# Kernel tuning notes

Measured on AMD Instinct MI355X. Metric: run time of the kernel, lower is better.

The kernel has to match this reference:

```python
import jax, jax.numpy as jnp
import numpy as np

B, A, G, C = 64, 8732, 50, 81
NEG_POS_RATIO = 3


def _make_boxes(key, b, n):
    k1, k2 = jax.random.split(key)
    mins = jax.random.uniform(k1, (b, n, 2)) * 0.7
    sizes = jax.random.uniform(k2, (b, n, 2)) * 0.3 + 0.01
    return jnp.concatenate([mins, mins + sizes], axis=-1)  # [b,n,4] xyxy


def setup_inputs() -> dict:
    key = jax.random.key(0)
    k1, k2, k3, k4 = jax.random.split(key, 4)
    pred_boxes = _make_boxes(k1, B, A)
    gt_boxes = _make_boxes(k2, B, G)
    pred_scores = jax.random.normal(k3, (B, A, C), dtype=jnp.float32)
    gt_labels = jax.random.randint(k4, (B, G), 0, C)
    return {"pred_boxes": pred_boxes, "pred_scores": pred_scores,
            "gt_boxes": gt_boxes, "gt_labels": gt_labels}


def _iou(a, b):
    # a: [B,A,4], b: [B,G,4] -> [B,A,G]
    a_ = a[:, :, None, :]
    b_ = b[:, None, :, :]
    iw = jnp.clip(jnp.minimum(a_[..., 2], b_[..., 2]) - jnp.maximum(a_[..., 0], b_[..., 0]), 0)
    ih = jnp.clip(jnp.minimum(a_[..., 3], b_[..., 3]) - jnp.maximum(a_[..., 1], b_[..., 1]), 0)
    inter = iw * ih
    area_a = (a_[..., 2] - a_[..., 0]) * (a_[..., 3] - a_[..., 1])
    area_b = (b_[..., 2] - b_[..., 0]) * (b_[..., 3] - b_[..., 1])
    union = jnp.clip(area_a + area_b - inter, 1e-6)
    return inter / union


def reference(pred_boxes, pred_scores, gt_boxes, gt_labels):
    num_anchors = pred_boxes.shape[1]
    iou = _iou(pred_boxes, gt_boxes)              # [B,A,G]
    best_iou = iou.max(axis=2)                    # [B,A]
    best_idx = iou.argmax(axis=2)                 # [B,A]
    pos = best_iou > 0.5

    matched_boxes = jnp.take_along_axis(gt_boxes, best_idx[..., None], axis=1)   # [B,A,4]
    matched_labels = jnp.take_along_axis(gt_labels, best_idx, axis=1)            # [B,A]
    target_boxes = jnp.where(pos[..., None], matched_boxes, 0.0)
    target_labels = jnp.where(pos, matched_labels, 0)

    pos_mask = target_labels > 0
    num_pos = pos_mask.sum(axis=1)                # [B]

    # smooth L1 (beta=1), summed over box coords
    d = pred_boxes - target_boxes
    ad = jnp.abs(d)
    sl1 = jnp.where(ad < 1.0, 0.5 * d * d, ad - 0.5).sum(axis=2)  # [B,A]
    loc_loss = (sl1 * pos_mask).sum()

    # cross entropy per anchor
    log_p = jax.nn.log_softmax(pred_scores, axis=-1)
    conf = -jnp.take_along_axis(log_p, target_labels[..., None], axis=-1)[..., 0]  # [B,A]

    conf_pos = (conf * pos_mask).sum()

    # hard negative mining: top (3*num_pos) losses among negatives
    conf_neg = jnp.where(pos_mask, -1.0, conf)
    num_neg = jnp.minimum(NEG_POS_RATIO * num_pos, num_anchors - 1)   # [B]
    order = jnp.argsort(-conf_neg, axis=1)        # descending
    rank = jnp.argsort(order, axis=1)             # rank of each anchor in sorted order
    hard_neg = rank < num_neg[:, None]
    conf_neg_hard = (conf * hard_neg).sum()

    total = (loc_loss + conf_pos + conf_neg_hard) / jnp.maximum(num_pos, 1).sum()
    return total
```

## Files before the change

kernel.cpp:

```cpp
#include <hip/hip_runtime.h>

#define BB 64
#define AA 8732
#define GG 50
#define CC 81
#define NEG_RATIO 3
#define HW 16
#define HSTRIDE 257
#define NCHUNK 137
#define XB 27


__device__ __forceinline__ unsigned mono_key(float f) {
    unsigned u = __float_as_uint(f);
    u = (u & 0x80000000u) ? ~u : (u | 0x80000000u);
    return ~u;
}

__device__ __forceinline__ float unkey_val(unsigned key) {
    unsigned u = ~key;
    return __uint_as_float((u & 0x80000000u) ? (u & 0x7fffffffu) : ~u);
}

__global__ __launch_bounds__(256, 5) void k_match(
    const float* __restrict__ pred_boxes, const float* __restrict__ pred_scores,
    const float* __restrict__ gt_boxes, const int* __restrict__ gt_labels,
    float* __restrict__ confneg_out,
    float* __restrict__ acc_slots, int* __restrict__ np_slots,
    unsigned* __restrict__ ctr)
{
    __shared__ float4 sgt[GG];
    __shared__ float  sarea[GG];
    __shared__ int    slab[GG];
    __shared__ float  redf[4];
    __shared__ int    redi[4];

    const int tid = threadIdx.x;
    const int b = blockIdx.y;
    const int x = blockIdx.x;
    const int grp = tid >> 2;
    const int q   = tid & 3;

    if (b == 0 && x == 0 && tid == 0) *ctr = 0u;

    if (tid < GG) {
        float4 g4 = ((const float4*)gt_boxes)[b * GG + tid];
        sgt[tid] = g4;
        sarea[tid] = (g4.z - g4.x) * (g4.w - g4.y);
        slab[tid] = gt_labels[b * GG + tid];
    }
    __syncthreads();

    const float*  sb = pred_scores + (size_t)b * AA * CC;
    const float4* bbx = (const float4*)pred_boxes + (size_t)b * AA;

    float contrib = 0.f;
    int npos = 0;

    const int a0 = x * 64 + grp;
    float4 cbox = bbx[a0];
    const float* crow = sb + (size_t)a0 * CC;
    float psum;
    {
        const float4 v0 = *(const float4*)(crow + 4 * q);
        const float4 v1 = *(const float4*)(crow + 4 * q + 16);
        const float4 v2 = *(const float4*)(crow + 4 * q + 32);
        const float4 v3 = *(const float4*)(crow + 4 * q + 48);
        const float4 v4 = *(const float4*)(crow + 4 * q + 64);
        const float  v80 = crow[80];
        float ps = 0.f;
        ps += __expf(v0.x) + __expf(v0.y) + __expf(v0.z) + __expf(v0.w);
        ps += __expf(v1.x) + __expf(v1.y) + __expf(v1.z) + __expf(v1.w);
        ps += __expf(v2.x) + __expf(v2.y) + __expf(v2.z) + __expf(v2.w);
        ps += __expf(v3.x) + __expf(v3.y) + __expf(v3.z) + __expf(v3.w);
        ps += __expf(v4.x) + __expf(v4.y) + __expf(v4.z) + __expf(v4.w);
        if (q == 0) ps += __expf(v80);
        psum = ps;
    }

    for (int c = x; c < NCHUNK; c += XB) {
        const int a = c * 64 + grp;
        const bool valid = a < AA;

        int cnx = c + XB; if (cnx >= NCHUNK) cnx = c;
        int an = cnx * 64 + grp; if (an >= AA) an = AA - 1;
        const float4 nbox = bbx[an];
        const float* nrow = sb + (size_t)an * CC;
        const float4 n0 = *(const float4*)(nrow + 4 * q);
        const float4 n1 = *(const float4*)(nrow + 4 * q + 16);
        const float4 n2 = *(const float4*)(nrow + 4 * q + 32);
        const float4 n3 = *(const float4*)(nrow + 4 * q + 48);
        const float4 n4 = *(const float4*)(nrow + 4 * q + 64);
        const float  n80 = nrow[80];

        const float4 pb = cbox;
        const float area_p = (pb.z - pb.x) * (pb.w - pb.y);
        float best = -1.f; int bidx = 0x7fffffff;
        #pragma unroll
        for (int i = 0; i < 13; ++i) {
            const int g = q + (i << 2);
            const bool gv = g < GG;
            const int gc = gv ? g : 0;
            const float4 gb = sgt[gc];
            const float  sa = sarea[gc];
            float iw = fmaxf(fminf(pb.z, gb.z) - fmaxf(pb.x, gb.x), 0.f);
            float ih = fmaxf(fminf(pb.w, gb.w) - fmaxf(pb.y, gb.y), 0.f);
            float inter = iw * ih;
            float uni = fmaxf(area_p + sa - inter, 1e-6f);
            float iou = __fdividef(inter, uni);
            if (gv && iou > best) { best = iou; bidx = g; }
        }
        #pragma unroll
        for (int off = 1; off < 4; off <<= 1) {
            float ov = __shfl_xor(best, off);
            int   oi = __shfl_xor(bidx, off);
            if (ov > best || (ov == best && oi < bidx)) { best = ov; bidx = oi; }
        }
        const int label = (best > 0.5f) ? slab[bidx] : 0;

        const float labv = crow[label];

        float sm = psum;
        sm += __shfl_xor(sm, 1);
        sm += __shfl_xor(sm, 2);

        if (q == 0 && valid) {
            const float conf = __logf(sm) - labv;
            const size_t ai = (size_t)b * AA + a;
            const bool pm = label > 0;
            confneg_out[ai] = pm ? -1.f : conf;
            if (pm) {
                npos++;
                const float4 gb = sgt[bidx];
                float sl1 = 0.f, d, ad;
                d = pb.x - gb.x; ad = fabsf(d); sl1 += (ad < 1.f) ? 0.5f * d * d : ad - 0.5f;
                d = pb.y - gb.y; ad = fabsf(d); sl1 += (ad < 1.f) ? 0.5f * d * d : ad - 0.5f;
                d = pb.z - gb.z; ad = fabsf(d); sl1 += (ad < 1.f) ? 0.5f * d * d : ad - 0.5f;
                d = pb.w - gb.w; ad = fabsf(d); sl1 += (ad < 1.f) ? 0.5f * d * d : ad - 0.5f;
                contrib += sl1 + conf;
            }
        }

        float ps = 0.f;
        ps += __expf(n0.x) + __expf(n0.y) + __expf(n0.z) + __expf(n0.w);
        ps += __expf(n1.x) + __expf(n1.y) + __expf(n1.z) + __expf(n1.w);
        ps += __expf(n2.x) + __expf(n2.y) + __expf(n2.z) + __expf(n2.w);
        ps += __expf(n3.x) + __expf(n3.y) + __expf(n3.z) + __expf(n3.w);
        ps += __expf(n4.x) + __expf(n4.y) + __expf(n4.z) + __expf(n4.w);
        if (q == 0) ps += __expf(n80);

        cbox = nbox; crow = nrow; psum = ps;
    }

    #pragma unroll
    for (int off = 32; off; off >>= 1) {
        contrib += __shfl_down(contrib, off);
        npos    += __shfl_down(npos, off);
    }
    const int wv = tid >> 6;
    if ((tid & 63) == 0) { redf[wv] = contrib; redi[wv] = npos; }
    __syncthreads();
    if (tid == 0) {
        acc_slots[b * XB + x] = redf[0] + redf[1] + redf[2] + redf[3];
        np_slots[b * XB + x]  = redi[0] + redi[1] + redi[2] + redi[3];
    }
}

__global__ __launch_bounds__(1024) void k_hardneg(
    const float* __restrict__ confneg,
    const int* __restrict__ np_slots, const float* __restrict__ acc_slots,
    float* __restrict__ per_b, int* __restrict__ den_b,
    unsigned* __restrict__ ctr, float* __restrict__ out)
{
    __shared__ unsigned hist[HW * HSTRIDE];
    __shared__ unsigned binsum[256];
    __shared__ unsigned sel[2];
    __shared__ unsigned uE[HW], uG[HW], eb[HW];
    __shared__ float    fred[HW];
    __shared__ int      stot;
    __shared__ int      slast;

    const int b = blockIdx.x;
    const int tid = threadIdx.x;
    const int wv = tid >> 6;
    const int lane = tid & 63;

    int np = 0;
    #pragma unroll
    for (int i = 0; i < XB; ++i) np += np_slots[b * XB + i];
    int k = NEG_RATIO * np; if (k > AA - 1) k = AA - 1;

    float hn = 0.f;
    if (k > 0) {
        const float* cn = confneg + (size_t)b * AA;

        const int lo = tid * 9;
        int nk = AA - lo; nk = nk > 9 ? 9 : (nk < 0 ? 0 : nk);
        unsigned keys[9];
        #pragma unroll
        for (int j = 0; j < 9; ++j)
            if (j < nk) keys[j] = mono_key(cn[lo + j]);

        unsigned prefix = 0, kk = (unsigned)k;
        for (int lev = 0; lev < 4; ++lev) {
            const int shift = 24 - 8 * lev;
            for (int i = tid; i < HW * HSTRIDE; i += 1024) hist[i] = 0;
            __syncthreads();
            #pragma unroll
            for (int j = 0; j < 9; ++j) {
                if (j < nk) {
                    const unsigned key = keys[j];
                    if (lev == 0 || (key >> (shift + 8)) == prefix)
                        atomicAdd(&hist[wv * HSTRIDE + ((key >> shift) & 255u)], 1u);
                }
            }
            __syncthreads();
            if (tid < 256) {
                unsigned s = 0;
                #pragma unroll
                for (int w = 0; w < HW; ++w) s += hist[w * HSTRIDE + tid];
                binsum[tid] = s;
            }
            __syncthreads();
            if (wv == 0) {
                const unsigned v0 = binsum[4 * lane], v1 = binsum[4 * lane + 1];
                const unsigned v2 = binsum[4 * lane + 2], v3 = binsum[4 * lane + 3];
                const unsigned lsum = v0 + v1 + v2 + v3;
                unsigned sc = lsum;
                #pragma unroll
                for (int off = 1; off < 64; off <<= 1) {
                    unsigned t = __shfl_up(sc, off);
                    if (lane >= off) sc += t;
                }
                const unsigned excl = sc - lsum;
                if (kk > excl && kk <= sc) {
                    unsigned cacc = excl;
                    if (kk <= cacc + v0)              { sel[0] = 4 * lane;     sel[1] = kk - cacc; }
                    else if (kk <= (cacc += v0) + v1) { sel[0] = 4 * lane + 1; sel[1] = kk - cacc; }
                    else if (kk <= (cacc += v1) + v2) { sel[0] = 4 * lane + 2; sel[1] = kk - cacc; }
                    else                              { sel[0] = 4 * lane + 3; sel[1] = kk - cacc - v2; }
                }
            }
            __syncthreads();
            prefix = (prefix << 8) | sel[0];
            kk = sel[1];
        }
        const unsigned kth = prefix;

        int cntG = 0, cntE = 0; float sum_gt = 0.f;
        #pragma unroll
        for (int j = 0; j < 9; ++j) {
            if (j < nk) {
                if (keys[j] < kth)       { cntG++; sum_gt += unkey_val(keys[j]); }
                else if (keys[j] == kth) { cntE++; }
            }
        }
        int sc = cntE;
        #pragma unroll
        for (int off = 1; off < 64; off <<= 1) {
            int t = __shfl_up(sc, off);
            if (lane >= off) sc += t;
        }
        int gt = cntG;
        #pragma unroll
        for (int off = 32; off; off >>= 1) gt += __shfl_down(gt, off);
        if (lane == 63) uE[wv] = (unsigned)sc;
        if (lane == 0)  uG[wv] = (unsigned)gt;
        __syncthreads();
        if (wv == 0) {
            unsigned e = (lane < HW) ? uE[lane] : 0u;
            unsigned g = (lane < HW) ? uG[lane] : 0u;
            unsigned se = e;
            #pragma unroll
            for (int off = 1; off < 16; off <<= 1) {
                unsigned t = __shfl_up(se, off);
                if (lane >= off) se += t;
            }
            if (lane < HW) eb[lane] = se - e;
            #pragma unroll
            for (int off = 8; off; off >>= 1) g += __shfl_down(g, off);
            if (lane == 0) stot = (int)g;
        }
        __syncthreads();
        const int m = k - stot;
        const int exclE = (int)eb[wv] + (sc - cntE);

        float sum_eq = 0.f;
        if (m > 0 && cntE > 0) {
            int seen = 0;
            #pragma unroll
            for (int j = 0; j < 9; ++j) {
                if (j < nk && keys[j] == kth) {
                    if (exclE + seen < m) sum_eq += unkey_val(keys[j]);
                    seen++;
                }
            }
        }

        float contrib = sum_gt + sum_eq;
        #pragma unroll
        for (int off = 32; off; off >>= 1) contrib += __shfl_down(contrib, off);
        if (lane == 0) fred[wv] = contrib;
        __syncthreads();
        if (tid == 0) {
            #pragma unroll
            for (int w = 0; w < HW; ++w) hn += fred[w];
        }
    }

    if (tid == 0) {
        float accb = 0.f;
        #pragma unroll
        for (int i = 0; i < XB; ++i) accb += acc_slots[b * XB + i];
        atomicExch(&per_b[b], accb + hn);
        atomicExch(&den_b[b], np > 1 ? np : 1);
        __threadfence();
        unsigned prev = atomicAdd(ctr, 1u);
        slast = (prev == (unsigned)(BB - 1)) ? 1 : 0;
    }
    __syncthreads();
    if (slast && tid < BB) {
        float v = atomicAdd(&per_b[tid], 0.f);
        int   d = atomicAdd(&den_b[tid], 0);
        #pragma unroll
        for (int off = 32; off; off >>= 1) {
            v += __shfl_down(v, off);
            d += __shfl_down(d, off);
        }
        if (tid == 0) out[0] = v / (float)d;
    }
}

extern "C" void kernel_launch(void* const* d_in, const int* in_sizes, int n_in,
                              void* d_out, int out_size, void* d_ws, size_t ws_size,
                              hipStream_t stream) {
    const float* pred_boxes  = (const float*)d_in[0];
    const float* pred_scores = (const float*)d_in[1];
    const float* gt_boxes    = (const float*)d_in[2];
    const int*   gt_labels   = (const int*)d_in[3];

    float*    ws        = (float*)d_ws;
    float*    acc_slots = ws;
    int*      np_slots  = (int*)(ws + 2048);
    float*    per_b     = ws + 4096;
    int*      den_b     = (int*)(ws + 4160);
    unsigned* ctr       = (unsigned*)(ws + 4224);
    float*    conf_neg  = ws + 8192;

    dim3 g1(XB, BB);
    k_match<<<g1, 256, 0, stream>>>(pred_boxes, pred_scores, gt_boxes, gt_labels,
                                    conf_neg, acc_slots, np_slots, ctr);
    k_hardneg<<<BB, 1024, 0, stream>>>(conf_neg, np_slots, acc_slots,
                                       per_b, den_b, ctr, (float*)d_out);
}
```

Measured before the change: 348.4 us.

## Split fused match kernel into separate log-sum-exp and IoU-matching kernels

Replaces the persistent, software-pipelined match kernel with two kernels. The first computes per-anchor log-sum-exp over the 81 classes with one block per 64-anchor chunk across the whole grid, storing it alongside the class-0 score. The second does IoU matching with one thread per anchor over all 50 ground-truth boxes, reading the stored LSE and gathering the label score only for positives. The aim is more parallelism and less register pressure per kernel, at the cost of an extra launch and a round trip of the intermediate LSE array through memory.

```diff
diff --git a/kernel.cpp b/kernel.cpp
--- a/kernel.cpp
+++ b/kernel.cpp
@@ -7,8 +7,7 @@
 #define NEG_RATIO 3
 #define HW 16
 #define HSTRIDE 257
-#define NCHUNK 137
-#define XB 27
+#define NXB 35
 
 
 __device__ __forceinline__ unsigned mono_key(float f) {
@@ -22,12 +21,51 @@
     return __uint_as_float((u & 0x80000000u) ? (u & 0x7fffffffu) : ~u);
 }
 
-__global__ __launch_bounds__(256, 5) void k_match(
+__global__ __launch_bounds__(256) void k_expsum(
+    const float* __restrict__ pred_scores,
+    float2* __restrict__ lse_s0, unsigned* __restrict__ ctr)
+{
+    const int tid = threadIdx.x;
+    const int b = blockIdx.y;
+    const int x = blockIdx.x;
+    const int grp = tid >> 2;
+    const int q   = tid & 3;
+
+    if (b == 0 && x == 0 && tid == 0) *ctr = 0u;
+
+    const int a = x * 64 + grp;
+    const int am = a < AA ? a : AA - 1;
+    const float* row = pred_scores + ((size_t)b * AA + am) * CC;
+
+    const float4 v0 = *(const float4*)(row + 4 * q);
+    const float4 v1 = *(const float4*)(row + 4 * q + 16);
+    const float4 v2 = *(const float4*)(row + 4 * q + 32);
+    const float4 v3 = *(const float4*)(row + 4 * q + 48);
+    const float4 v4 = *(const float4*)(row + 4 * q + 64);
+    const float  v80 = row[80];
+
+    float ps = 0.f;
+    ps += __expf(v0.x) + __expf(v0.y) + __expf(v0.z) + __expf(v0.w);
+    ps += __expf(v1.x) + __expf(v1.y) + __expf(v1.z) + __expf(v1.w);
+    ps += __expf(v2.x) + __expf(v2.y) + __expf(v2.z) + __expf(v2.w);
+    ps += __expf(v3.x) + __expf(v3.y) + __expf(v3.z) + __expf(v3.w);
+    ps += __expf(v4.x) + __expf(v4.y) + __expf(v4.z) + __expf(v4.w);
+    if (q == 0) ps += __expf(v80);
+
+    float sm = ps;
+    sm += __shfl_xor(sm, 1);
+    sm += __shfl_xor(sm, 2);
+
+    if (q == 0 && a < AA)
+        lse_s0[(size_t)b * AA + a] = make_float2(__logf(sm), v0.x);
+}
+
+__global__ __launch_bounds__(256) void k_iou(
     const float* __restrict__ pred_boxes, const float* __restrict__ pred_scores,
     const float* __restrict__ gt_boxes, const int* __restrict__ gt_labels,
+    const float2* __restrict__ lse_s0,
     float* __restrict__ confneg_out,
-    float* __restrict__ acc_slots, int* __restrict__ np_slots,
-    unsigned* __restrict__ ctr)
+    float* __restrict__ acc_slots, int* __restrict__ np_slots)
 {
     __shared__ float4 sgt[GG];
     __shared__ float  sarea[GG];
@@ -38,10 +76,6 @@
     const int tid = threadIdx.x;
     const int b = blockIdx.y;
     const int x = blockIdx.x;
-    const int grp = tid >> 2;
-    const int q   = tid & 3;
-
-    if (b == 0 && x == 0 && tid == 0) *ctr = 0u;
 
     if (tid < GG) {
         float4 g4 = ((const float4*)gt_boxes)[b * GG + tid];
@@ -51,105 +85,43 @@
     }
     __syncthreads();
 
-    const float*  sb = pred_scores + (size_t)b * AA * CC;
-    const float4* bbx = (const float4*)pred_boxes + (size_t)b * AA;
-
+    const int a = x * 256 + tid;
     float contrib = 0.f;
     int npos = 0;
 
-    const int a0 = x * 64 + grp;
-    float4 cbox = bbx[a0];
-    const float* crow = sb + (size_t)a0 * CC;
-    float psum;
-    {
-        const float4 v0 = *(const float4*)(crow + 4 * q);
-        const float4 v1 = *(const float4*)(crow + 4 * q + 16);
-        const float4 v2 = *(const float4*)(crow + 4 * q + 32);
-        const float4 v3 = *(const float4*)(crow + 4 * q + 48);
-        const float4 v4 = *(const float4*)(crow + 4 * q + 64);
-        const float  v80 = crow[80];
-        float ps = 0.f;
-        ps += __expf(v0.x) + __expf(v0.y) + __expf(v0.z) + __expf(v0.w);
-        ps += __expf(v1.x) + __expf(v1.y) + __expf(v1.z) + __expf(v1.w);
-        ps += __expf(v2.x) + __expf(v2.y) + __expf(v2.z) + __expf(v2.w);
-        ps += __expf(v3.x) + __expf(v3.y) + __expf(v3.z) + __expf(v3.w);
-        ps += __expf(v4.x) + __expf(v4.y) + __expf(v4.z) + __expf(v4.w);
-        if (q == 0) ps += __expf(v80);
-        psum = ps;
-    }
-
-    for (int c = x; c < NCHUNK; c += XB) {
-        const int a = c * 64 + grp;
-        const bool valid = a < AA;
-
-        int cnx = c + XB; if (cnx >= NCHUNK) cnx = c;
-        int an = cnx * 64 + grp; if (an >= AA) an = AA - 1;
-        const float4 nbox = bbx[an];
-        const float* nrow = sb + (size_t)an * CC;
-        const float4 n0 = *(const float4*)(nrow + 4 * q);
-        const float4 n1 = *(const float4*)(nrow + 4 * q + 16);
-        const float4 n2 = *(const float4*)(nrow + 4 * q + 32);
-        const float4 n3 = *(const float4*)(nrow + 4 * q + 48);
-        const float4 n4 = *(const float4*)(nrow + 4 * q + 64);
-        const float  n80 = nrow[80];
-
-        const float4 pb = cbox;
+    if (a < AA) {
+        const float4 pb = ((const float4*)pred_boxes)[(size_t)b * AA + a];
         const float area_p = (pb.z - pb.x) * (pb.w - pb.y);
-        float best = -1.f; int bidx = 0x7fffffff;
-        #pragma unroll
-        for (int i = 0; i < 13; ++i) {
-            const int g = q + (i << 2);
-            const bool gv = g < GG;
-            const int gc = gv ? g : 0;
-            const float4 gb = sgt[gc];
-            const float  sa = sarea[gc];
+        float best = -1.f; int bidx = 0;
+        #pragma unroll
+        for (int g = 0; g < GG; ++g) {
+            const float4 gb = sgt[g];
+            const float  sa = sarea[g];
             float iw = fmaxf(fminf(pb.z, gb.z) - fmaxf(pb.x, gb.x), 0.f);
             float ih = fmaxf(fminf(pb.w, gb.w) - fmaxf(pb.y, gb.y), 0.f);
             float inter = iw * ih;
             float uni = fmaxf(area_p + sa - inter, 1e-6f);
             float iou = __fdividef(inter, uni);
-            if (gv && iou > best) { best = iou; bidx = g; }
-        }
-        #pragma unroll
-        for (int off = 1; off < 4; off <<= 1) {
-            float ov = __shfl_xor(best, off);
-            int   oi = __shfl_xor(bidx, off);
-            if (ov > best || (ov == best && oi < bidx)) { best = ov; bidx = oi; }
+            if (iou > best) { best = iou; bidx = g; }
         }
         const int label = (best > 0.5f) ? slab[bidx] : 0;
 
-        const float labv = crow[label];
-
-        float sm = psum;
-        sm += __shfl_xor(sm, 1);
-        sm += __shfl_xor(sm, 2);
-
-        if (q == 0 && valid) {
-            const float conf = __logf(sm) - labv;
-            const size_t ai = (size_t)b * AA + a;
-            const bool pm = label > 0;
-            confneg_out[ai] = pm ? -1.f : conf;
-            if (pm) {
-                npos++;
-                const float4 gb = sgt[bidx];
-                float sl1 = 0.f, d, ad;
-                d = pb.x - gb.x; ad = fabsf(d); sl1 += (ad < 1.f) ? 0.5f * d * d : ad - 0.5f;
-                d = pb.y - gb.y; ad = fabsf(d); sl1 += (ad < 1.f) ? 0.5f * d * d : ad - 0.5f;
-                d = pb.z - gb.z; ad = fabsf(d); sl1 += (ad < 1.f) ? 0.5f * d * d : ad - 0.5f;
-                d = pb.w - gb.w; ad = fabsf(d); sl1 += (ad < 1.f) ? 0.5f * d * d : ad - 0.5f;
-                contrib += sl1 + conf;
-            }
-        }
-
-        float ps = 0.f;
-        ps += __expf(n0.x) + __expf(n0.y) + __expf(n0.z) + __expf(n0.w);
-        ps += __expf(n1.x) + __expf(n1.y) + __expf(n1.z) + __expf(n1.w);
-        ps += __expf(n2.x) + __expf(n2.y) + __expf(n2.z) + __expf(n2.w);
-        ps += __expf(n3.x) + __expf(n3.y) + __expf(n3.z) + __expf(n3.w);
-        ps += __expf(n4.x) + __expf(n4.y) + __expf(n4.z) + __expf(n4.w);
-        if (q == 0) ps += __expf(n80);
-
-        cbox = nbox; crow = nrow; psum = ps;
+        const float2 ls = lse_s0[(size_t)b * AA + a];
+        const float labv = (label == 0) ? ls.y
+                         : pred_scores[((size_t)b * AA + a) * CC + label];
+        const float conf = ls.x - labv;
+        const bool pm = label > 0;
+        confneg_out[(size_t)b * AA + a] = pm ? -1.f : conf;
+        if (pm) {
+            npos++;
+            const float4 gb = sgt[bidx];
+            float sl1 = 0.f, d, ad;
+            d = pb.x - gb.x; ad = fabsf(d); sl1 += (ad < 1.f) ? 0.5f * d * d : ad - 0.5f;
+            d = pb.y - gb.y; ad = fabsf(d); sl1 += (ad < 1.f) ? 0.5f * d * d : ad - 0.5f;
+            d = pb.z - gb.z; ad = fabsf(d); sl1 += (ad < 1.f) ? 0.5f * d * d : ad - 0.5f;
+            d = pb.w - gb.w; ad = fabsf(d); sl1 += (ad < 1.f) ? 0.5f * d * d : ad - 0.5f;
+            contrib += sl1 + conf;
+        }
     }
 
     #pragma unroll
@@ -161,8 +133,8 @@
     if ((tid & 63) == 0) { redf[wv] = contrib; redi[wv] = npos; }
     __syncthreads();
     if (tid == 0) {
-        acc_slots[b * XB + x] = redf[0] + redf[1] + redf[2] + redf[3];
-        np_slots[b * XB + x]  = redi[0] + redi[1] + redi[2] + redi[3];
+        acc_slots[b * NXB + x] = redf[0] + redf[1] + redf[2] + redf[3];
+        np_slots[b * NXB + x]  = redi[0] + redi[1] + redi[2] + redi[3];
     }
 }
 
@@ -187,7 +159,7 @@
 
     int np = 0;
     #pragma unroll
-    for (int i = 0; i < XB; ++i) np += np_slots[b * XB + i];
+    for (int i = 0; i < NXB; ++i) np += np_slots[b * NXB + i];
     int k = NEG_RATIO * np; if (k > AA - 1) k = AA - 1;
 
     float hn = 0.f;
@@ -311,7 +283,7 @@
     if (tid == 0) {
         float accb = 0.f;
         #pragma unroll
-        for (int i = 0; i < XB; ++i) accb += acc_slots[b * XB + i];
+        for (int i = 0; i < NXB; ++i) accb += acc_slots[b * NXB + i];
         atomicExch(&per_b[b], accb + hn);
         atomicExch(&den_b[b], np > 1 ? np : 1);
         __threadfence();
@@ -341,15 +313,18 @@
 
     float*    ws        = (float*)d_ws;
     float*    acc_slots = ws;
-    int*      np_slots  = (int*)(ws + 2048);
-    float*    per_b     = ws + 4096;
-    int*      den_b     = (int*)(ws + 4160);
-    unsigned* ctr       = (unsigned*)(ws + 4224);
-    float*    conf_neg  = ws + 8192;
-
-    dim3 g1(XB, BB);
-    k_match<<<g1, 256, 0, stream>>>(pred_boxes, pred_scores, gt_boxes, gt_labels,
-                                    conf_neg, acc_slots, np_slots, ctr);
+    int*      np_slots  = (int*)(ws + 4096);
+    float*    per_b     = ws + 8192;
+    int*      den_b     = (int*)(ws + 8256);
+    unsigned* ctr       = (unsigned*)(ws + 8320);
+    float*    conf_neg  = ws + 16384;
+    float2*   lse_s0    = (float2*)(ws + 16384 + 561152);
+
+    dim3 gA(137, BB);
+    k_expsum<<<gA, 256, 0, stream>>>(pred_scores, lse_s0, ctr);
+    dim3 gB(NXB, BB);
+    k_iou<<<gB, 256, 0, stream>>>(pred_boxes, pred_scores, gt_boxes, gt_labels,
+                                  lse_s0, conf_neg, acc_slots, np_slots);
     k_hardneg<<<BB, 1024, 0, stream>>>(conf_neg, np_slots, acc_slots,
                                        per_b, den_b, ctr, (float*)d_out);
 }
```

Result: faster. 303.5 us (-12.9%).
